# Optimization experiments

Hardware: AMD Instinct MI355X
Metric: run time of the kernel (lower is better)

The kernel has to match this reference:

```python
import jax, jax.numpy as jnp
import numpy as np

B, N, D_IN, D_OUT, K_NBR = 8, 2048, 128, 128, 8
BN_EPS = 1e-5

def setup_inputs() -> dict:
    key = jax.random.key(0)
    ks = jax.random.split(key, 5)
    xavier = (6.0 / (D_IN + D_OUT)) ** 0.5
    return {
        "x": jax.random.normal(ks[0], (B, N, D_IN), jnp.float32),
        "weight_self": jax.random.uniform(ks[1], (D_IN, D_OUT), jnp.float32, -xavier, xavier),
        "weight_neighbor": jax.random.uniform(ks[2], (D_IN, D_OUT), jnp.float32, -xavier, xavier),
        "kan_a": jax.random.normal(ks[3], (D_OUT, 3), jnp.float32) * 0.1,
        "kan_b": jax.random.normal(ks[4], (D_OUT, 2), jnp.float32) * 0.1,
        "bias": jnp.zeros((D_OUT,), jnp.float32),
        "bn_gamma": jnp.ones((D_OUT,), jnp.float32),
        "bn_beta": jnp.zeros((D_OUT,), jnp.float32),
    }

def _forward(x, weight_self, weight_neighbor, kan_a, kan_b, bias, bn_gamma, bn_beta):
    b, n, _ = x.shape
    # --- kNN graph build ---
    xx = jnp.sum(x * x, axis=2, keepdims=True)                       # [B,N,1]
    dist = xx - 2.0 * jnp.einsum('bnd,bmd->bnm', x, x) + jnp.swapaxes(xx, 1, 2)
    dist = jnp.clip(dist, 0.0, None)                                  # [B,N,N]
    k = min(K_NBR + 1, n)
    _, idx = jax.lax.top_k(-dist, k)                                  # smallest-k indices
    nbr = idx[:, :, 1:]                                               # drop self, [B,N,k-1]
    adj = jnp.zeros((b, n, n), x.dtype).at[
        jnp.arange(b)[:, None, None], jnp.arange(n)[None, :, None], nbr
    ].set(1.0)
    deg_inv_sqrt = (jnp.sum(adj, axis=2) + 1e-6) ** -0.5              # [B,N]
    adj_norm = deg_inv_sqrt[:, :, None] * adj * deg_inv_sqrt[:, None, :]
    adj_norm = adj_norm + jnp.eye(n, dtype=x.dtype)[None]
    # --- graph conv ---
    h_self = x @ weight_self                                          # [B,N,F]
    h_nbr = jnp.einsum('bnm,bmf->bnf', adj_norm, x @ weight_neighbor)
    h = h_self + h_nbr + bias
    # --- rational KAN activation (per-channel coefficients) ---
    h2 = h * h
    num = kan_a[:, 0] + kan_a[:, 1] * h + kan_a[:, 2] * h2
    den = 1.0 + jnp.abs(kan_b[:, 0] * h + kan_b[:, 1] * h2)
    h = num / (den + 1e-8)
    # --- BatchNorm1d (training mode): normalize each channel over (B,N) ---
    mean = jnp.mean(h, axis=(0, 1))
    var = jnp.var(h, axis=(0, 1))                                     # biased, matches torch BN
    h = (h - mean) * jax.lax.rsqrt(var + BN_EPS) * bn_gamma + bn_beta
    return h

def reference(x, weight_self, weight_neighbor, kan_a, kan_b, bias, bn_gamma, bn_beta):
    return _forward(x, weight_self, weight_neighbor, kan_a, kan_b, bias, bn_gamma, bn_beta)
```

## Files before the change

### kernel.cpp

```cpp
#include <hip/hip_runtime.h>
#include <stdint.h>

#define BB 8
#define NN 2048
#define DD 128

typedef unsigned long long ull;
typedef unsigned int u32;
typedef unsigned short u16;
typedef __attribute__((ext_vector_type(8))) short bf16x8;
typedef __attribute__((ext_vector_type(4))) float f32x4;

#define INS8(t8, cand) do { \
    t8[7] = (cand); ull _t; \
    if (t8[7] < t8[6]) { _t = t8[6]; t8[6] = t8[7]; t8[7] = _t; } \
    if (t8[6] < t8[5]) { _t = t8[5]; t8[5] = t8[6]; t8[6] = _t; } \
    if (t8[5] < t8[4]) { _t = t8[4]; t8[4] = t8[5]; t8[5] = _t; } \
    if (t8[4] < t8[3]) { _t = t8[3]; t8[3] = t8[4]; t8[4] = _t; } \
    if (t8[3] < t8[2]) { _t = t8[2]; t8[2] = t8[3]; t8[3] = _t; } \
    if (t8[2] < t8[1]) { _t = t8[1]; t8[1] = t8[2]; t8[2] = _t; } \
    if (t8[1] < t8[0]) { _t = t8[0]; t8[0] = t8[1]; t8[1] = _t; } \
  } while (0)

#define LADDER8(s8, cd) do { \
    u32 _c = (cd); \
    _Pragma("unroll") \
    for (int _s = 0; _s < 8; ++_s) { \
      u32 _lo = (s8[_s] <= _c) ? s8[_s] : _c; \
      u32 _hi = (s8[_s] <= _c) ? _c : s8[_s]; \
      s8[_s] = _lo; _c = _hi; \
    } } while (0)

__device__ inline u16 f2bf_rn(float f) {
  uint32_t u = __float_as_uint(f);
  return (u16)((u + 0x7fffu + ((u >> 16) & 1u)) >> 16);
}

typedef __attribute__((address_space(1))) const void gvoid_t;
typedef __attribute__((address_space(3))) void lvoid_t;
__device__ __forceinline__ void gload16(const void* g, void* l) {
  __builtin_amdgcn_global_load_lds((gvoid_t*)g, (lvoid_t*)l, 16, 0, 0);
}

__global__ __launch_bounds__(256) void k_cvx(const float* __restrict__ x,
                                             float* __restrict__ xx,
                                             u16* __restrict__ xh,
                                             u16* __restrict__ xl) {
  int row  = blockIdx.x * 4 + (threadIdx.x >> 6);
  int lane = threadIdx.x & 63;
  float2 v = *reinterpret_cast<const float2*>(x + (size_t)row * DD + lane * 2);
  float p = v.x * v.x + v.y * v.y;
  #pragma unroll
  for (int off = 1; off < 64; off <<= 1) p += __shfl_xor(p, off);
  if (lane == 0) xx[row] = p;
  u16 h0 = f2bf_rn(v.x);
  u16 l0 = f2bf_rn(v.x - __uint_as_float(((uint32_t)h0) << 16));
  u16 h1 = f2bf_rn(v.y);
  u16 l1 = f2bf_rn(v.y - __uint_as_float(((uint32_t)h1) << 16));
  size_t o = (size_t)row * DD + lane * 2;
  *(uint32_t*)(xh + o) = (uint32_t)h0 | ((uint32_t)h1 << 16);
  *(uint32_t*)(xl + o) = (uint32_t)l0 | ((uint32_t)l1 << 16);
}

__global__ __launch_bounds__(256, 2) void k_gemm(const float* __restrict__ x,
                                                 const float* __restrict__ Ws,
                                                 const float* __restrict__ Wn,
                                                 const float* __restrict__ bias,
                                                 float* __restrict__ hbase,
                                                 float* __restrict__ y) {
  __shared__ __align__(16) float xt[128 * 64];
  __shared__ __align__(16) float wt[128 * 64];
  int tid = threadIdx.x;
  int ch = blockIdx.x & 1;
  size_t r0 = (size_t)(blockIdx.x >> 1) * 64;

  {
    int rr = tid >> 2, kp = (tid & 3) << 5;
    const float* src = x + (r0 + rr) * DD + kp;
    #pragma unroll
    for (int q = 0; q < 8; ++q) {
      float4 v = *(const float4*)(src + (q << 2));
      int k = kp + (q << 2);
      xt[(k + 0) * 64 + rr] = v.x; xt[(k + 1) * 64 + rr] = v.y;
      xt[(k + 2) * 64 + rr] = v.z; xt[(k + 3) * 64 + rr] = v.w;
    }
  }
  {
    const float4* s4 = (const float4*)Ws;
    float4* w4 = (float4*)wt;
    #pragma unroll
    for (int q = 0; q < 8; ++q) {
      int idx = q * 256 + tid;
      w4[idx] = s4[((idx >> 4) << 5) + (ch << 4) + (idx & 15)];
    }
  }
  __syncthreads();

  int tc = tid & 15, tr = tid >> 4;
  float accS[4][4], accY[4][4];
  #pragma unroll
  for (int i = 0; i < 4; ++i)
    #pragma unroll
    for (int u = 0; u < 4; ++u) { accS[i][u] = 0.f; accY[i][u] = 0.f; }

  #pragma unroll 4
  for (int k = 0; k < 128; ++k) {
    float4 a4 = *(const float4*)(xt + k * 64 + (tr << 2));
    float4 w4 = *(const float4*)(wt + k * 64 + (tc << 2));
    float aa[4] = {a4.x, a4.y, a4.z, a4.w};
    float ww[4] = {w4.x, w4.y, w4.z, w4.w};
    #pragma unroll
    for (int i = 0; i < 4; ++i)
      #pragma unroll
      for (int u = 0; u < 4; ++u) accS[i][u] = fmaf(aa[i], ww[u], accS[i][u]);
  }
  __syncthreads();
  {
    const float4* s4 = (const float4*)Wn;
    float4* w4 = (float4*)wt;
    #pragma unroll
    for (int q = 0; q < 8; ++q) {
      int idx = q * 256 + tid;
      w4[idx] = s4[((idx >> 4) << 5) + (ch << 4) + (idx & 15)];
    }
  }
  __syncthreads();
  #pragma unroll 4
  for (int k = 0; k < 128; ++k) {
    float4 a4 = *(const float4*)(xt + k * 64 + (tr << 2));
    float4 w4 = *(const float4*)(wt + k * 64 + (tc << 2));
    float aa[4] = {a4.x, a4.y, a4.z, a4.w};
    float ww[4] = {w4.x, w4.y, w4.z, w4.w};
    #pragma unroll
    for (int i = 0; i < 4; ++i)
      #pragma unroll
      for (int u = 0; u < 4; ++u) accY[i][u] = fmaf(aa[i], ww[u], accY[i][u]);
  }

  int cg = (ch << 6) + (tc << 2);
  float4 bv = *(const float4*)(bias + cg);
  float bb[4] = {bv.x, bv.y, bv.z, bv.w};
  #pragma unroll
  for (int i = 0; i < 4; ++i) {
    size_t row = r0 + (tr << 2) + i;
    float h[4];
    #pragma unroll
    for (int u = 0; u < 4; ++u) h[u] = (accS[i][u] + accY[i][u]) + bb[u];
    *(float4*)(y + row * DD + cg)     = make_float4(accY[i][0], accY[i][1], accY[i][2], accY[i][3]);
    *(float4*)(hbase + row * DD + cg) = make_float4(h[0], h[1], h[2], h[3]);
  }
}

#define GLOAD(MC, BUF) do { \
    _Pragma("unroll") \
    for (int q = 0; q < 4; ++q) { \
      int ks_ = ((q & 1) << 2) + sks; \
      int mrow_ = mbase + ((MC) << 5) + ((q >> 1) << 4) + sr; \
      const u16* src_ = (ks_ < 4 ? xhb : xlb) + ((size_t)mrow_ << 7) + ((ks_ & 3) << 5) + (sg << 3); \
      gload16(src_, (char*)(&Bc[(BUF)][0]) + (((q << 8) + tid) << 4)); \
    } } while (0)

__global__ __launch_bounds__(256, 4) void k_knn(const u16* __restrict__ xh,
                                                const u16* __restrict__ xl,
                                                const float* __restrict__ xx,
                                                u32* __restrict__ cand) {
  __shared__ __align__(16) u16 Bc[2][8192];
  __shared__ float xxm[512];

  int tid = threadIdx.x;
  int lane = tid & 63, w = tid >> 6;
  int b = blockIdx.x & 7;
  int rest = blockIdx.x >> 3;
  int n0 = (rest & 31) << 6;
  int msplit = rest >> 5;
  int mbase = msplit << 9;
  const u16*  xhb = xh + (((size_t)b << 11) << 7);
  const u16*  xlb = xl + (((size_t)b << 11) << 7);
  const float* xxb = xx + ((size_t)b << 11);

  int sr = tid & 15, sg = (tid >> 4) & 3, sks = (tid >> 6) & 3;

  GLOAD(0, 0);

  {
    float2 t = *(const float2*)(xxb + mbase + tid * 2);
    xxm[tid * 2] = t.x; xxm[tid * 2 + 1] = t.y;
  }

  int r = lane & 15, g = lane >> 4;
  int myn = n0 + (w << 4) + r;
  float xxn = xxb[myn];

  bf16x8 ah[4], al[4];
  #pragma unroll
  for (int ks = 0; ks < 4; ++ks) {
    ah[ks] = *(const bf16x8*)(xhb + ((size_t)myn << 7) + (ks << 5) + (g << 3));
    al[ks] = *(const bf16x8*)(xlb + ((size_t)myn << 7) + (ks << 5) + (g << 3));
  }

  u32 t8[8];
  #pragma unroll
  for (int q = 0; q < 8; ++q) t8[q] = 0xFFFFFFFFu;

  __syncthreads();

  int cur = 0;
  for (int mc = 0; mc < 16; ++mc) {
    if (mc < 15) GLOAD(mc + 1, cur ^ 1);
    const u16* Bcur = &Bc[cur][0];
    #pragma unroll
    for (int p = 0; p < 2; ++p) {
      f32x4 ahh = {0.f, 0.f, 0.f, 0.f};
      f32x4 alh = {0.f, 0.f, 0.f, 0.f};
      f32x4 ahl = {0.f, 0.f, 0.f, 0.f};
      #pragma unroll
      for (int ks = 0; ks < 4; ++ks) {
        const u16* base = Bcur + (((p << 3) + ks) << 9) + (lane << 3);
        bf16x8 bh = *(const bf16x8*)(base);
        bf16x8 bo = *(const bf16x8*)(base + 2048);
        ahh = __builtin_amdgcn_mfma_f32_16x16x32_bf16(bh, ah[ks], ahh, 0, 0, 0);
        alh = __builtin_amdgcn_mfma_f32_16x16x32_bf16(bo, ah[ks], alh, 0, 0, 0);
        ahl = __builtin_amdgcn_mfma_f32_16x16x32_bf16(bh, al[ks], ahl, 0, 0, 0);
      }
      float4 xm4 = *(const float4*)(xxm + (mc << 5) + (p << 4) + (g << 2));
      float sx[4] = {xxn + xm4.x, xxn + xm4.y, xxn + xm4.z, xxn + xm4.w};
      int mb0 = mbase + (mc << 5) + (p << 4) + (g << 2);
      #pragma unroll
      for (int e = 0; e < 4; ++e) {
        float dot = (ahh[e] + alh[e]) + ahl[e];
        float d = fmaxf(fmaf(-2.f, dot, sx[e]), 0.f);
        int m = mb0 + e;
        u32 cd = (__float_as_uint(d) & 0xFFFFF000u) | (u32)m;
        cd = (m == myn) ? 0xFFFFFFFFu : cd;
        LADDER8(t8, cd);
      }
    }
    __syncthreads();
    cur ^= 1;
  }

  u32* mbuf = (u32*)(&Bc[0][0]);
  #pragma unroll
  for (int q = 0; q < 8; ++q)
    mbuf[((((w << 4) + r) << 5)) + (g << 3) + q] = t8[q];
  __syncthreads();
  if (g == 0) {
    for (int j = 1; j < 4; ++j) {
      #pragma unroll
      for (int q = 0; q < 8; ++q) {
        u32 cd = mbuf[((((w << 4) + r) << 5)) + (j << 3) + q];
        LADDER8(t8, cd);
      }
    }
    u32* cp = cand + ((((size_t)b << 11) + myn) << 5) + (msplit << 3);
    #pragma unroll
    for (int q = 0; q < 8; ++q) cp[q] = t8[q];
  }
}

__global__ __launch_bounds__(256) void k_rsc(const float* __restrict__ x,
                                             const float* __restrict__ xx,
                                             const u32* __restrict__ cand,
                                             int* __restrict__ nbr) {
  __shared__ ull ex[256];
  int tid = threadIdx.x;
  int rloc = tid >> 5;
  int c = tid & 31;
  int row = blockIdx.x * 8 + rloc;
  int b = row >> 11;
  u32 cd32 = cand[((size_t)row << 5) + c];
  int m = (int)(cd32 & 0xFFFu);
  const float* xn = x + (size_t)row * DD;
  const float* xm = x + ((size_t)(b << 11) + m) * DD;
  float acc = 0.f;
  #pragma unroll
  for (int d4 = 0; d4 < 32; ++d4) {
    float4 a = *(const float4*)(xn + (d4 << 2));
    float4 v = *(const float4*)(xm + (d4 << 2));
    acc = fmaf(a.x, v.x, acc);
    acc = fmaf(a.y, v.y, acc);
    acc = fmaf(a.z, v.z, acc);
    acc = fmaf(a.w, v.w, acc);
  }
  float dist = fmaxf((xx[row] - 2.f * acc) + xx[(b << 11) + m], 0.f);
  ex[tid] = (((ull)__float_as_uint(dist)) << 32) | (unsigned)m;
  __syncthreads();
  if (c == 0) {
    ull t8[8];
    #pragma unroll
    for (int q = 0; q < 8; ++q) t8[q] = ~0ull;
    #pragma unroll
    for (int q = 0; q < 32; ++q) {
      ull v = ex[(rloc << 5) + q];
      if (v < t8[7]) INS8(t8, v);
    }
    int* op = nbr + (size_t)row * 8;
    #pragma unroll
    for (int q = 0; q < 8; ++q) op[q] = (int)(t8[q] & 0xffffffffu);
  }
}

__global__ __launch_bounds__(256) void k_kan(const float* __restrict__ hbase,
                                             const float* __restrict__ y,
                                             const int* __restrict__ nbr,
                                             const float* __restrict__ kan_a,
                                             const float* __restrict__ kan_b,
                                             float* __restrict__ hkan,
                                             double* __restrict__ sums) {
  __shared__ double redA[256], redB[256];
  int f = threadIdx.x & 127;
  int half = threadIdx.x >> 7;
  int r0 = blockIdx.x * 32 + half * 16;
  int bb = r0 >> 11;
  const float* yb = y + ((size_t)bb << 11) * DD;
  float a0 = kan_a[f * 3 + 0], a1 = kan_a[f * 3 + 1], a2 = kan_a[f * 3 + 2];
  float b0 = kan_b[f * 2 + 0], b1 = kan_b[f * 2 + 1];
  float disf = (float)(1.0 / sqrt((double)(8.0f + 1e-6f)));
  float cf = disf * disf;
  double sh = 0.0, sh2 = 0.0;
  for (int i = 0; i < 16; ++i) {
    int r = r0 + i;
    const int* np_ = nbr + (size_t)r * 8;
    float t = 0.f;
    #pragma unroll
    for (int j = 0; j < 8; ++j) {
      int m = np_[j];
      float yv = yb[(size_t)m * DD + f];
      t = fmaf(cf, yv, t);
    }
    float h = hbase[(size_t)r * DD + f] + t;
    float h2 = h * h;
    float num = (a0 + a1 * h) + a2 * h2;
    float den = 1.0f + fabsf(b0 * h + b1 * h2);
    float hk = num / (den + 1e-8f);
    hkan[(size_t)r * DD + f] = hk;
    sh += (double)hk; sh2 += (double)hk * (double)hk;
  }
  redA[threadIdx.x] = sh; redB[threadIdx.x] = sh2;
  __syncthreads();
  if (half == 0) {
    atomicAdd(&sums[f], sh + redA[f + 128]);
    atomicAdd(&sums[128 + f], sh2 + redB[f + 128]);
  }
}

__global__ __launch_bounds__(256) void k_bn(const float* __restrict__ hkan,
                                            const double* __restrict__ sums,
                                            const float* __restrict__ gamma,
                                            const float* __restrict__ beta,
                                            float* __restrict__ out) {
  __shared__ float mn[128], sc[128], bt[128];
  int tid = threadIdx.x;
  if (tid < 128) {
    double M = (double)(BB * NN);
    double mean = sums[tid] / M;
    double var = sums[128 + tid] / M - mean * mean;
    if (var < 0.0) var = 0.0;
    mn[tid] = (float)mean;
    sc[tid] = (float)(1.0 / sqrt(var + 1e-5)) * gamma[tid];
    bt[tid] = beta[tid];
  }
  __syncthreads();
  const int total4 = BB * NN * DD / 4;
  for (int i4 = blockIdx.x * blockDim.x + threadIdx.x; i4 < total4;
       i4 += gridDim.x * blockDim.x) {
    float4 v = ((const float4*)hkan)[i4];
    int fb = (i4 * 4) & 127;
    float4 o;
    o.x = (v.x - mn[fb + 0]) * sc[fb + 0] + bt[fb + 0];
    o.y = (v.y - mn[fb + 1]) * sc[fb + 1] + bt[fb + 1];
    o.z = (v.z - mn[fb + 2]) * sc[fb + 2] + bt[fb + 2];
    o.w = (v.w - mn[fb + 3]) * sc[fb + 3] + bt[fb + 3];
    ((float4*)out)[i4] = o;
  }
}

extern "C" void kernel_launch(void* const* d_in, const int* in_sizes, int n_in,
                              void* d_out, int out_size, void* d_ws, size_t ws_size,
                              hipStream_t stream) {
  const float* x     = (const float*)d_in[0];
  const float* Ws    = (const float*)d_in[1];
  const float* Wn    = (const float*)d_in[2];
  const float* ka    = (const float*)d_in[3];
  const float* kb    = (const float*)d_in[4];
  const float* bias  = (const float*)d_in[5];
  const float* gamma = (const float*)d_in[6];
  const float* beta  = (const float*)d_in[7];
  float* out = (float*)d_out;

  char* ws = (char*)d_ws;
  float*  xx    = (float*)(ws + 0);
  int*    nbr   = (int*)(ws + 65536);
  double* sums  = (double*)(ws + 589824);
  float*  y     = (float*)(ws + 1048576);
  float*  hbase = (float*)(ws + 9437184);
  float*  hkan  = (float*)(ws + 17825792);
  u32*    cand  = (u32*)(ws + 17825792);
  u16*    xh    = (u16*)(ws + 22020096);
  u16*    xl    = (u16*)d_out;

  hipMemsetAsync(sums, 0, 256 * sizeof(double), stream);
  k_cvx <<<4096, 256, 0, stream>>>(x, xx, xh, xl);
  k_gemm<<<512,  256, 0, stream>>>(x, Ws, Wn, bias, hbase, y);
  k_knn <<<1024, 256, 0, stream>>>(xh, xl, xx, cand);
  k_rsc <<<2048, 256, 0, stream>>>(x, xx, cand, nbr);
  k_kan <<<512,  256, 0, stream>>>(hbase, y, nbr, ka, kb, hkan, sums);
  k_bn  <<<1024, 256, 0, stream>>>(hkan, sums, gamma, beta, out);
}
```

Measured before the change: 160.8 us.

## Use sorting-network merges for top-8, interleave batches across blocks, split dot accumulators

Each 8 distance candidates per chunk are now sorted with a sorting network and bitonic-merged into the running top-8, replacing per-candidate insertion ladders. The cross-lane reduction uses the same merge. In the rescoring and KAN kernels, block indices are remapped so consecutive blocks cover different batches. The rescoring dot product now uses 8 independent accumulators to shorten the FMA dependency chain, which slightly changes the floating-point summation order.

Result: faster. 149.2 us (-7.2%).

```diff
diff --git a/kernel.cpp b/kernel.cpp
--- a/kernel.cpp
+++ b/kernel.cpp
@@ -22,14 +22,32 @@
     if (t8[1] < t8[0]) { _t = t8[0]; t8[0] = t8[1]; t8[1] = _t; } \
   } while (0)
 
-#define LADDER8(s8, cd) do { \
-    u32 _c = (cd); \
-    _Pragma("unroll") \
-    for (int _s = 0; _s < 8; ++_s) { \
-      u32 _lo = (s8[_s] <= _c) ? s8[_s] : _c; \
-      u32 _hi = (s8[_s] <= _c) ? _c : s8[_s]; \
-      s8[_s] = _lo; _c = _hi; \
-    } } while (0)
+#define CEX(a, b) do { u32 _lo = (a) < (b) ? (a) : (b); \
+                       u32 _hi = (a) < (b) ? (b) : (a); \
+                       (a) = _lo; (b) = _hi; } while (0)
+
+#define SORT8(c) do { \
+    CEX(c[0], c[1]); CEX(c[2], c[3]); CEX(c[0], c[2]); CEX(c[1], c[3]); CEX(c[1], c[2]); \
+    CEX(c[4], c[5]); CEX(c[6], c[7]); CEX(c[4], c[6]); CEX(c[5], c[7]); CEX(c[5], c[6]); \
+    CEX(c[0], c[4]); CEX(c[1], c[5]); CEX(c[2], c[6]); CEX(c[3], c[7]); \
+    CEX(c[2], c[4]); CEX(c[3], c[5]); \
+    CEX(c[1], c[2]); CEX(c[3], c[4]); CEX(c[5], c[6]); } while (0)
+
+#define MERGE8(t, s) do { \
+    u32 m0_ = (t)[0] < (s)[7] ? (t)[0] : (s)[7]; \
+    u32 m1_ = (t)[1] < (s)[6] ? (t)[1] : (s)[6]; \
+    u32 m2_ = (t)[2] < (s)[5] ? (t)[2] : (s)[5]; \
+    u32 m3_ = (t)[3] < (s)[4] ? (t)[3] : (s)[4]; \
+    u32 m4_ = (t)[4] < (s)[3] ? (t)[4] : (s)[3]; \
+    u32 m5_ = (t)[5] < (s)[2] ? (t)[5] : (s)[2]; \
+    u32 m6_ = (t)[6] < (s)[1] ? (t)[6] : (s)[1]; \
+    u32 m7_ = (t)[7] < (s)[0] ? (t)[7] : (s)[0]; \
+    CEX(m0_, m4_); CEX(m1_, m5_); CEX(m2_, m6_); CEX(m3_, m7_); \
+    CEX(m0_, m2_); CEX(m1_, m3_); CEX(m4_, m6_); CEX(m5_, m7_); \
+    CEX(m0_, m1_); CEX(m2_, m3_); CEX(m4_, m5_); CEX(m6_, m7_); \
+    (t)[0] = m0_; (t)[1] = m1_; (t)[2] = m2_; (t)[3] = m3_; \
+    (t)[4] = m4_; (t)[5] = m5_; (t)[6] = m6_; (t)[7] = m7_; \
+  } while (0)
 
 __device__ inline u16 f2bf_rn(float f) {
   uint32_t u = __float_as_uint(f);
@@ -208,6 +226,7 @@
   for (int mc = 0; mc < 16; ++mc) {
     if (mc < 15) GLOAD(mc + 1, cur ^ 1);
     const u16* Bcur = &Bc[cur][0];
+    u32 cds[8];
     #pragma unroll
     for (int p = 0; p < 2; ++p) {
       f32x4 ahh = {0.f, 0.f, 0.f, 0.f};
@@ -231,10 +250,11 @@
         float d = fmaxf(fmaf(-2.f, dot, sx[e]), 0.f);
         int m = mb0 + e;
         u32 cd = (__float_as_uint(d) & 0xFFFFF000u) | (u32)m;
-        cd = (m == myn) ? 0xFFFFFFFFu : cd;
-        LADDER8(t8, cd);
+        cds[(p << 2) + e] = (m == myn) ? 0xFFFFFFFFu : cd;
       }
     }
+    SORT8(cds);
+    MERGE8(t8, cds);
     __syncthreads();
     cur ^= 1;
   }
@@ -246,11 +266,11 @@
   __syncthreads();
   if (g == 0) {
     for (int j = 1; j < 4; ++j) {
+      u32 s8[8];
       #pragma unroll
-      for (int q = 0; q < 8; ++q) {
-        u32 cd = mbuf[((((w << 4) + r) << 5)) + (j << 3) + q];
-        LADDER8(t8, cd);
-      }
+      for (int q = 0; q < 8; ++q)
+        s8[q] = mbuf[((((w << 4) + r) << 5)) + (j << 3) + q];
+      MERGE8(t8, s8);
     }
     u32* cp = cand + ((((size_t)b << 11) + myn) << 5) + (msplit << 3);
     #pragma unroll
@@ -266,23 +286,32 @@
   int tid = threadIdx.x;
   int rloc = tid >> 5;
   int c = tid & 31;
-  int row = blockIdx.x * 8 + rloc;
-  int b = row >> 11;
+  int batch = blockIdx.x & 7;
+  int within = blockIdx.x >> 3;
+  int row = (batch << 11) + (within << 3) + rloc;
   u32 cd32 = cand[((size_t)row << 5) + c];
   int m = (int)(cd32 & 0xFFFu);
   const float* xn = x + (size_t)row * DD;
-  const float* xm = x + ((size_t)(b << 11) + m) * DD;
-  float acc = 0.f;
-  #pragma unroll
-  for (int d4 = 0; d4 < 32; ++d4) {
-    float4 a = *(const float4*)(xn + (d4 << 2));
-    float4 v = *(const float4*)(xm + (d4 << 2));
-    acc = fmaf(a.x, v.x, acc);
-    acc = fmaf(a.y, v.y, acc);
-    acc = fmaf(a.z, v.z, acc);
-    acc = fmaf(a.w, v.w, acc);
-  }
-  float dist = fmaxf((xx[row] - 2.f * acc) + xx[(b << 11) + m], 0.f);
+  const float* xm = x + ((size_t)(batch << 11) + m) * DD;
+  float acc[8] = {0.f, 0.f, 0.f, 0.f, 0.f, 0.f, 0.f, 0.f};
+  #pragma unroll
+  for (int d8 = 0; d8 < 16; ++d8) {
+    float4 a0 = *(const float4*)(xn + (d8 << 3));
+    float4 a1 = *(const float4*)(xn + (d8 << 3) + 4);
+    float4 v0 = *(const float4*)(xm + (d8 << 3));
+    float4 v1 = *(const float4*)(xm + (d8 << 3) + 4);
+    acc[0] = fmaf(a0.x, v0.x, acc[0]);
+    acc[1] = fmaf(a0.y, v0.y, acc[1]);
+    acc[2] = fmaf(a0.z, v0.z, acc[2]);
+    acc[3] = fmaf(a0.w, v0.w, acc[3]);
+    acc[4] = fmaf(a1.x, v1.x, acc[4]);
+    acc[5] = fmaf(a1.y, v1.y, acc[5]);
+    acc[6] = fmaf(a1.z, v1.z, acc[6]);
+    acc[7] = fmaf(a1.w, v1.w, acc[7]);
+  }
+  float dot = ((acc[0] + acc[1]) + (acc[2] + acc[3])) +
+              ((acc[4] + acc[5]) + (acc[6] + acc[7]));
+  float dist = fmaxf((xx[row] - 2.f * dot) + xx[(batch << 11) + m], 0.f);
   ex[tid] = (((ull)__float_as_uint(dist)) << 32) | (unsigned)m;
   __syncthreads();
   if (c == 0) {
@@ -310,9 +339,10 @@
   __shared__ double redA[256], redB[256];
   int f = threadIdx.x & 127;
   int half = threadIdx.x >> 7;
-  int r0 = blockIdx.x * 32 + half * 16;
-  int bb = r0 >> 11;
-  const float* yb = y + ((size_t)bb << 11) * DD;
+  int batch = blockIdx.x & 7;
+  int within = blockIdx.x >> 3;
+  int r0 = (batch << 11) + (within << 5) + half * 16;
+  const float* yb = y + ((size_t)batch << 11) * DD;
   float a0 = kan_a[f * 3 + 0], a1 = kan_a[f * 3 + 1], a2 = kan_a[f * 3 + 2];
   float b0 = kan_b[f * 2 + 0], b1 = kan_b[f * 2 + 1];
   float disf = (float)(1.0 / sqrt((double)(8.0f + 1e-6f)));
```
